# Kernel optimization log

Measured on AMD Instinct MI355X. Metric: run time of the kernel, lower is better.

The kernel has to match this reference:

```python
import jax, jax.numpy as jnp
import numpy as np

B, IN, H = 4096, 2048, 2048


def setup_inputs() -> dict:
    key = jax.random.key(0)
    ks = jax.random.split(key, 20)
    s_in = 1.0 / np.sqrt(IN)
    s_h = 1.0 / np.sqrt(H)
    inp = {
        "x": jax.random.normal(ks[0], (B, IN), jnp.float32),
        "h": jax.random.normal(ks[1], (B, H), jnp.float32),
        "c": jax.random.normal(ks[2], (B, H), jnp.float32),
    }
    names_in = [("Wii", "bii"), ("Wif", "bif"), ("Wig", "big"), ("Wio", "bio")]
    names_h = [("Whi", "bhi"), ("Whf", "bhf"), ("Whg", "bhg"), ("Who", "bho")]
    k = 3
    for wn, bn in names_in:
        inp[wn] = jax.random.normal(ks[k], (H, IN), jnp.float32) * s_in
        inp[bn] = jax.random.normal(ks[k + 1], (H,), jnp.float32) * s_in
        k += 2
    for wn, bn in names_h:
        inp[wn] = jax.random.normal(ks[k], (H, H), jnp.float32) * s_h
        inp[bn] = jax.random.normal(ks[k + 1], (H,), jnp.float32) * s_h
        k += 2
    return inp


def reference(x, h, c, Wii, bii, Whi, bhi, Wif, bif, Whf, bhf,
              Wig, big, Whg, bhg, Wio, bio, Who, bho):
    # Fuse the 4 input-projections and 4 hidden-projections into two GEMMs
    # (same math as 8 separate nn.Linear calls).
    Wx = jnp.concatenate([Wii, Wif, Wig, Wio], axis=0)   # [4H, IN]
    Wh = jnp.concatenate([Whi, Whf, Whg, Who], axis=0)   # [4H, H]
    bx = jnp.concatenate([bii, bif, big, bio])            # [4H]
    bh = jnp.concatenate([bhi, bhf, bhg, bho])            # [4H]
    gates = x @ Wx.T + h @ Wh.T + bx + bh                 # [B, 4H]
    ii, ff, gg, oo = jnp.split(gates, 4, axis=-1)
    i = jax.nn.sigmoid(ii)
    f = jax.nn.sigmoid(ff)
    g = jnp.tanh(gg)
    o = jax.nn.sigmoid(oo)
    c_new = f * c + i * g
    h_new = o * jnp.tanh(c_new)
    return jnp.stack([h_new, c_new])  # [2, B, H]
```

## Files before the change

kernel.cpp:

```cpp
#include <hip/hip_runtime.h>
#include <stdint.h>

typedef __attribute__((ext_vector_type(4))) float f32x4;
typedef __attribute__((ext_vector_type(8))) short bf16x8;

#define MFMA_BF16 __builtin_amdgcn_mfma_f32_16x16x32_bf16

__device__ __forceinline__ unsigned short f2bf(float f) {
  union { float f; uint32_t u; } a; a.f = f;
  uint32_t u = a.u;
  uint32_t r = (u + 0x7FFFu + ((u >> 16) & 1u)) >> 16;
  return (unsigned short)r;
}

__global__ void pack_a_kernel(const float4* __restrict__ x, const float4* __restrict__ hh,
                              ushort4* __restrict__ A) {
  const int total = 4096 * 1024;
  for (int q = blockIdx.x * blockDim.x + threadIdx.x; q < total; q += gridDim.x * blockDim.x) {
    int row = q >> 10, cq = q & 1023;
    float4 v = (cq < 512) ? x[row * 512 + cq] : hh[row * 512 + (cq - 512)];
    ushort4 o; o.x = f2bf(v.x); o.y = f2bf(v.y); o.z = f2bf(v.z); o.w = f2bf(v.w);
    A[q] = o;
  }
}

__global__ void pack_w_kernel(const float* __restrict__ Wii, const float* __restrict__ Wif,
                              const float* __restrict__ Wig, const float* __restrict__ Wio,
                              const float* __restrict__ Whi, const float* __restrict__ Whf,
                              const float* __restrict__ Whg, const float* __restrict__ Who,
                              ushort4* __restrict__ Wp) {
  const int total = 8192 * 1024;
  for (int q = blockIdx.x * blockDim.x + threadIdx.x; q < total; q += gridDim.x * blockDim.x) {
    int p = q >> 10, kq = q & 1023;
    int r = p & 255;
    int g = ((r >> 7) << 1) | ((r >> 4) & 1);
    int H = ((p >> 8) << 6) | (((r >> 5) & 3) << 4) | (r & 15);
    const float* src;
    if (kq < 512) src = (g == 0) ? Wii : (g == 1) ? Wif : (g == 2) ? Wig : Wio;
    else          src = (g == 0) ? Whi : (g == 1) ? Whf : (g == 2) ? Whg : Who;
    const float4 v = *(const float4*)&src[(size_t)H * 2048 + ((kq & 511) << 2)];
    ushort4 o; o.x = f2bf(v.x); o.y = f2bf(v.y); o.z = f2bf(v.z); o.w = f2bf(v.w);
    Wp[q] = o;
  }
}

#define STG(srcbase, jj, koff, dstE)                                                        \
  __builtin_amdgcn_global_load_lds(                                                        \
      (const __attribute__((address_space(1))) void*)((srcbase) + (size_t)(jj)*262144 + (koff)), \
      (__attribute__((address_space(3))) void*)(&smem[(dstE) + (jj)*4096]), 16, 0, 0)

__global__ __launch_bounds__(512, 1)
void lstm_gemm_kernel(const ushort* __restrict__ A, const ushort* __restrict__ Wp,
                      const float* __restrict__ c,
                      const float* __restrict__ bii, const float* __restrict__ bif_,
                      const float* __restrict__ big_, const float* __restrict__ bio_,
                      const float* __restrict__ bhi, const float* __restrict__ bhf,
                      const float* __restrict__ bhg, const float* __restrict__ bho,
                      float* __restrict__ out) {
  __shared__ ushort smem[65536];
  const int tid = threadIdx.x;
  const int lane = tid & 63, w = tid >> 6;
  const int wm = w >> 2, wn = w & 3;

  const int bid = blockIdx.x;
  const int xcd = bid & 7, q = bid >> 3;
  const int bn = (xcd << 2) | (q >> 4);
  const int bm = q & 15;

  const int laneRow = lane & 15, lane16 = lane >> 4;
  const int lr7 = laneRow & 7;
  const int colE0 = (lane16 ^ lr7) << 3;
  const int colE1 = ((4 + lane16) ^ lr7) << 3;

  const int srow = w * 8 + (lane >> 3);
  const int chunkOff = ((lane & 7) ^ (lane >> 3)) << 3;
  const ushort* aSrc = A + (size_t)(bm * 256 + srow) * 4096 + chunkOff;
  const ushort* bSrc = Wp + (size_t)(bn * 256 + srow) * 4096 + chunkOff;
  const int aDstW = w * 512;
  const int bDstW = 16384 + w * 512;

  const int aBase = (wm * 64 + laneRow) * 64;
  const int bBase = 16384 + (wn * 32 + laneRow) * 64;

  f32x4 acc[8][4];
#pragma unroll
  for (int i = 0; i < 8; i++)
#pragma unroll
    for (int j = 0; j < 4; j++) acc[i][j] = (f32x4){0.f, 0.f, 0.f, 0.f};

  STG(aSrc, 0, 0, aDstW); STG(aSrc, 1, 0, aDstW);
  STG(bSrc, 0, 0, bDstW); STG(bSrc, 1, 0, bDstW);
  STG(bSrc, 2, 0, bDstW); STG(bSrc, 3, 0, bDstW);
  STG(aSrc, 2, 0, aDstW); STG(aSrc, 3, 0, aDstW);
  STG(aSrc, 0, 64, 32768 + aDstW); STG(aSrc, 1, 64, 32768 + aDstW);
  STG(bSrc, 0, 64, 32768 + bDstW); STG(bSrc, 1, 64, 32768 + bDstW);
  STG(bSrc, 2, 64, 32768 + bDstW); STG(bSrc, 3, 64, 32768 + bDstW);
  STG(aSrc, 2, 64, 32768 + aDstW); STG(aSrc, 3, 64, 32768 + aDstW);
  asm volatile("s_waitcnt vmcnt(12)" ::: "memory");
  __builtin_amdgcn_s_barrier();
  __builtin_amdgcn_sched_barrier(0);

#pragma unroll 1
  for (int T = 0; T < 64; ++T) {
    const int bufE = (T & 1) << 15;
    const int kS = (T + 2) << 6;
    const bool st = (T <= 61);
    bf16x8 af[4][2], bf[4][2];

#pragma unroll
    for (int m = 0; m < 4; ++m) {
      af[m][0] = *(const bf16x8*)&smem[bufE + aBase + m * 1024 + colE0];
      af[m][1] = *(const bf16x8*)&smem[bufE + aBase + m * 1024 + colE1];
    }
#pragma unroll
    for (int n = 0; n < 2; ++n) {
      bf[n][0] = *(const bf16x8*)&smem[bufE + bBase + n * 1024 + colE0];
      bf[n][1] = *(const bf16x8*)&smem[bufE + bBase + n * 1024 + colE1];
    }
    __builtin_amdgcn_s_barrier();
    asm volatile("s_waitcnt lgkmcnt(0)" ::: "memory");
    __builtin_amdgcn_sched_barrier(0);
    __builtin_amdgcn_s_setprio(1);
#pragma unroll
    for (int m = 0; m < 4; ++m)
#pragma unroll
      for (int n = 0; n < 2; ++n) {
        acc[m][n] = MFMA_BF16(af[m][0], bf[n][0], acc[m][n], 0, 0, 0);
        acc[m][n] = MFMA_BF16(af[m][1], bf[n][1], acc[m][n], 0, 0, 0);
      }
    __builtin_amdgcn_s_setprio(0);
    if (T != 63) asm volatile("s_waitcnt vmcnt(10)" ::: "memory");
    else         asm volatile("s_waitcnt vmcnt(2)" ::: "memory");
    __builtin_amdgcn_s_barrier();

#pragma unroll
    for (int n = 0; n < 2; ++n) {
      bf[2 + n][0] = *(const bf16x8*)&smem[bufE + bBase + 8192 + n * 1024 + colE0];
      bf[2 + n][1] = *(const bf16x8*)&smem[bufE + bBase + 8192 + n * 1024 + colE1];
    }
    if (st) {
      STG(aSrc, 0, kS, bufE + aDstW); STG(aSrc, 1, kS, bufE + aDstW);
      STG(bSrc, 0, kS, bufE + bDstW); STG(bSrc, 1, kS, bufE + bDstW);
    }
    __builtin_amdgcn_s_barrier();
    asm volatile("s_waitcnt lgkmcnt(0)" ::: "memory");
    __builtin_amdgcn_sched_barrier(0);
    __builtin_amdgcn_s_setprio(1);
#pragma unroll
    for (int m = 0; m < 4; ++m)
#pragma unroll
      for (int n = 0; n < 2; ++n) {
        acc[m][2 + n] = MFMA_BF16(af[m][0], bf[2 + n][0], acc[m][2 + n], 0, 0, 0);
        acc[m][2 + n] = MFMA_BF16(af[m][1], bf[2 + n][1], acc[m][2 + n], 0, 0, 0);
      }
    __builtin_amdgcn_s_setprio(0);
    if (T != 63) asm volatile("s_waitcnt vmcnt(12)" ::: "memory");
    else         asm volatile("s_waitcnt vmcnt(0)" ::: "memory");
    __builtin_amdgcn_s_barrier();

#pragma unroll
    for (int m = 0; m < 4; ++m) {
      af[m][0] = *(const bf16x8*)&smem[bufE + aBase + 8192 + m * 1024 + colE0];
      af[m][1] = *(const bf16x8*)&smem[bufE + aBase + 8192 + m * 1024 + colE1];
    }
    if (st) { STG(bSrc, 2, kS, bufE + bDstW); STG(bSrc, 3, kS, bufE + bDstW); }
    __builtin_amdgcn_s_barrier();
    asm volatile("s_waitcnt lgkmcnt(0)" ::: "memory");
    __builtin_amdgcn_sched_barrier(0);
    __builtin_amdgcn_s_setprio(1);
#pragma unroll
    for (int m = 0; m < 4; ++m)
#pragma unroll
      for (int n = 0; n < 2; ++n) {
        acc[4 + m][n] = MFMA_BF16(af[m][0], bf[n][0], acc[4 + m][n], 0, 0, 0);
        acc[4 + m][n] = MFMA_BF16(af[m][1], bf[n][1], acc[4 + m][n], 0, 0, 0);
      }
    __builtin_amdgcn_s_setprio(0);
    __builtin_amdgcn_s_barrier();

    if (st) { STG(aSrc, 2, kS, bufE + aDstW); STG(aSrc, 3, kS, bufE + aDstW); }
    __builtin_amdgcn_s_barrier();
    __builtin_amdgcn_s_setprio(1);
#pragma unroll
    for (int m = 0; m < 4; ++m)
#pragma unroll
      for (int n = 0; n < 2; ++n) {
        acc[4 + m][2 + n] = MFMA_BF16(af[m][0], bf[2 + n][0], acc[4 + m][2 + n], 0, 0, 0);
        acc[4 + m][2 + n] = MFMA_BF16(af[m][1], bf[2 + n][1], acc[4 + m][2 + n], 0, 0, 0);
      }
    __builtin_amdgcn_s_setprio(0);
    if (T < 63) {
      if (T != 62) asm volatile("s_waitcnt vmcnt(12)" ::: "memory");
      else         asm volatile("s_waitcnt vmcnt(4)" ::: "memory");
      __builtin_amdgcn_s_barrier();
      __builtin_amdgcn_sched_barrier(0);
    }
  }

  const int hcol = bn * 64 + wn * 16 + laneRow;
  const float bI = bii[hcol] + bhi[hcol];
  const float bF = bif_[hcol] + bhf[hcol];
  const float bG = big_[hcol] + bhg[hcol];
  const float bO = bio_[hcol] + bho[hcol];
#pragma unroll
  for (int mi = 0; mi < 8; ++mi) {
    const int rowBase = bm * 256 + (mi >> 2) * 128 + wm * 64 + (mi & 3) * 16 + lane16 * 4;
#pragma unroll
    for (int rr = 0; rr < 4; ++rr) {
      const int row = rowBase + rr;
      const float ii = acc[mi][0][rr] + bI;
      const float ff = acc[mi][1][rr] + bF;
      const float gg = acc[mi][2][rr] + bG;
      const float oo = acc[mi][3][rr] + bO;
      const float iv = 1.f / (1.f + __expf(-ii));
      const float fv = 1.f / (1.f + __expf(-ff));
      const float gv = tanhf(gg);
      const float ov = 1.f / (1.f + __expf(-oo));
      const float cv = c[(size_t)row * 2048 + hcol];
      const float cn = fv * cv + iv * gv;
      const float hn = ov * tanhf(cn);
      out[(size_t)row * 2048 + hcol] = hn;
      out[(size_t)8388608 + (size_t)row * 2048 + hcol] = cn;
    }
  }
}

extern "C" void kernel_launch(void* const* d_in, const int* in_sizes, int n_in,
                              void* d_out, int out_size, void* d_ws, size_t ws_size,
                              hipStream_t stream) {
  const float* x = (const float*)d_in[0];
  const float* h = (const float*)d_in[1];
  const float* c = (const float*)d_in[2];
  const float* Wii = (const float*)d_in[3];  const float* bii = (const float*)d_in[4];
  const float* Wif = (const float*)d_in[5];  const float* bif_ = (const float*)d_in[6];
  const float* Wig = (const float*)d_in[7];  const float* big_ = (const float*)d_in[8];
  const float* Wio = (const float*)d_in[9];  const float* bio_ = (const float*)d_in[10];
  const float* Whi = (const float*)d_in[11]; const float* bhi = (const float*)d_in[12];
  const float* Whf = (const float*)d_in[13]; const float* bhf = (const float*)d_in[14];
  const float* Whg = (const float*)d_in[15]; const float* bhg = (const float*)d_in[16];
  const float* Who = (const float*)d_in[17]; const float* bho = (const float*)d_in[18];

  ushort* Abf = (ushort*)d_ws;
  ushort* Wpk = Abf + (size_t)4096 * 4096;
  float* out = (float*)d_out;

  pack_a_kernel<<<2048, 256, 0, stream>>>((const float4*)x, (const float4*)h, (ushort4*)Abf);
  pack_w_kernel<<<2048, 256, 0, stream>>>(Wii, Wif, Wig, Wio, Whi, Whf, Whg, Who, (ushort4*)Wpk);
  lstm_gemm_kernel<<<512, 512, 0, stream>>>(Abf, Wpk, c,
                                            bii, bif_, big_, bio_, bhi, bhf, bhg, bho, out);
}
```

Baseline: 334.3 us.

## Software-pipeline LDS fragment reads across K-tiles with register double buffering

Restructures the main GEMM loop so the LDS reads for the next K-tile's first A/B fragments are issued during the current tile's later MFMA phases, using ping-pong register buffers and a 2x unrolled loop. Explicit lgkmcnt(0) waits and extra barriers between LDS reads and MFMAs are removed, relying on compiler-inserted waits, and vmcnt thresholds are retuned to the new global-load ordering. This aims to hide LDS latency behind matrix math and cut barrier stalls, at the cost of more live vector registers and tighter correctness reliance on barrier/vmcnt placement.

```diff
diff --git a/kernel.cpp b/kernel.cpp
--- a/kernel.cpp
+++ b/kernel.cpp
@@ -49,6 +49,87 @@
       (const __attribute__((address_space(1))) void*)((srcbase) + (size_t)(jj)*262144 + (koff)), \
       (__attribute__((address_space(3))) void*)(&smem[(dstE) + (jj)*4096]), 16, 0, 0)
 
+#define TILE_BODY(T_, bufE_, AF0c, BF01c, AF0n, BF01n)                                      \
+  {                                                                                         \
+    const int kS = ((T_) + 2) << 6;                                                         \
+    const bool st = (T_) <= 61;                                                             \
+    const bool rdn = (T_) < 63;                                                             \
+                 \
+    _Pragma("unroll") for (int n = 0; n < 2; ++n) {                                         \
+      bf23_[n][0] = *(const bf16x8*)&smem[(bufE_) + bBase + 8192 + n * 1024 + colE0];       \
+      bf23_[n][1] = *(const bf16x8*)&smem[(bufE_) + bBase + 8192 + n * 1024 + colE1];       \
+    }                                                                                       \
+    __builtin_amdgcn_s_setprio(1);                                                          \
+    _Pragma("unroll") for (int m = 0; m < 4; ++m)                                           \
+      _Pragma("unroll") for (int n = 0; n < 2; ++n) {                                       \
+        acc[m][n] = MFMA_BF16(AF0c[m][0], BF01c[n][0], acc[m][n], 0, 0, 0);                 \
+        acc[m][n] = MFMA_BF16(AF0c[m][1], BF01c[n][1], acc[m][n], 0, 0, 0);                 \
+      }                                                                                     \
+    __builtin_amdgcn_s_setprio(0);                                                          \
+    if ((T_) < 63) asm volatile("s_waitcnt vmcnt(8)" ::: "memory");                         \
+    else           asm volatile("s_waitcnt vmcnt(0)" ::: "memory");                         \
+    __builtin_amdgcn_sched_barrier(0);                                                      \
+    __builtin_amdgcn_s_barrier();                                                           \
+            \
+    _Pragma("unroll") for (int m = 0; m < 4; ++m) {                                         \
+      af1_[m][0] = *(const bf16x8*)&smem[(bufE_) + aBase + 8192 + m * 1024 + colE0];        \
+      af1_[m][1] = *(const bf16x8*)&smem[(bufE_) + aBase + 8192 + m * 1024 + colE1];        \
+    }                                                                                       \
+    if (st) {                                                                               \
+      STG(aSrc, 0, kS, (bufE_) + aDstW); STG(aSrc, 1, kS, (bufE_) + aDstW);                 \
+      STG(bSrc, 0, kS, (bufE_) + bDstW); STG(bSrc, 1, kS, (bufE_) + bDstW);                 \
+    }                                                                                       \
+    __builtin_amdgcn_s_setprio(1);                                                          \
+    _Pragma("unroll") for (int m = 0; m < 4; ++m)                                           \
+      _Pragma("unroll") for (int n = 0; n < 2; ++n) {                                       \
+        acc[m][2 + n] = MFMA_BF16(AF0c[m][0], bf23_[n][0], acc[m][2 + n], 0, 0, 0);         \
+        acc[m][2 + n] = MFMA_BF16(AF0c[m][1], bf23_[n][1], acc[m][2 + n], 0, 0, 0);         \
+      }                                                                                     \
+    __builtin_amdgcn_s_setprio(0);                                                          \
+    if ((T_) < 62)       asm volatile("s_waitcnt vmcnt(8)" ::: "memory");                   \
+    else if ((T_) == 62) asm volatile("s_waitcnt vmcnt(4)" ::: "memory");                   \
+    __builtin_amdgcn_sched_barrier(0);                                                      \
+    __builtin_amdgcn_s_barrier();                                                           \
+     \
+    if (rdn) {                                                                              \
+      _Pragma("unroll") for (int m = 0; m < 4; ++m) {                                       \
+        AF0n[m][0] = *(const bf16x8*)&smem[((bufE_) ^ 32768) + aBase + m * 1024 + colE0];   \
+        AF0n[m][1] = *(const bf16x8*)&smem[((bufE_) ^ 32768) + aBase + m * 1024 + colE1];   \
+      }                                                                                     \
+    }                                                                                       \
+    if (st) { STG(bSrc, 2, kS, (bufE_) + bDstW); STG(bSrc, 3, kS, (bufE_) + bDstW); }       \
+    __builtin_amdgcn_s_setprio(1);                                                          \
+    _Pragma("unroll") for (int m = 0; m < 4; ++m)                                           \
+      _Pragma("unroll") for (int n = 0; n < 2; ++n) {                                       \
+        acc[4 + m][n] = MFMA_BF16(af1_[m][0], BF01c[n][0], acc[4 + m][n], 0, 0, 0);         \
+        acc[4 + m][n] = MFMA_BF16(af1_[m][1], BF01c[n][1], acc[4 + m][n], 0, 0, 0);         \
+      }                                                                                     \
+    __builtin_amdgcn_s_setprio(0);                                                          \
+    __builtin_amdgcn_sched_barrier(0);                                                      \
+    __builtin_amdgcn_s_barrier();                                                           \
+           \
+    if (rdn) {                                                                              \
+      _Pragma("unroll") for (int n = 0; n < 2; ++n) {                                       \
+        BF01n[n][0] = *(const bf16x8*)&smem[((bufE_) ^ 32768) + bBase + n * 1024 + colE0];  \
+        BF01n[n][1] = *(const bf16x8*)&smem[((bufE_) ^ 32768) + bBase + n * 1024 + colE1];  \
+      }                                                                                     \
+    }                                                                                       \
+    if (st) { STG(aSrc, 2, kS, (bufE_) + aDstW); STG(aSrc, 3, kS, (bufE_) + aDstW); }       \
+    __builtin_amdgcn_s_setprio(1);                                                          \
+    _Pragma("unroll") for (int m = 0; m < 4; ++m)                                           \
+      _Pragma("unroll") for (int n = 0; n < 2; ++n) {                                       \
+        acc[4 + m][2 + n] = MFMA_BF16(af1_[m][0], bf23_[n][0], acc[4 + m][2 + n], 0, 0, 0); \
+        acc[4 + m][2 + n] = MFMA_BF16(af1_[m][1], bf23_[n][1], acc[4 + m][2 + n], 0, 0, 0); \
+      }                                                                                     \
+    __builtin_amdgcn_s_setprio(0);                                                          \
+    if ((T_) < 62)       asm volatile("s_waitcnt vmcnt(10)" ::: "memory");                  \
+    else if ((T_) == 62) asm volatile("s_waitcnt vmcnt(2)" ::: "memory");                   \
+    if ((T_) < 63) {                                                                        \
+      __builtin_amdgcn_sched_barrier(0);                                                    \
+      __builtin_amdgcn_s_barrier();                                                         \
+    }                                                                                       \
+  }
+
 __global__ __launch_bounds__(512, 1)
 void lstm_gemm_kernel(const ushort* __restrict__ A, const ushort* __restrict__ Wp,
                       const float* __restrict__ c,
@@ -96,105 +177,27 @@
   STG(bSrc, 0, 64, 32768 + bDstW); STG(bSrc, 1, 64, 32768 + bDstW);
   STG(bSrc, 2, 64, 32768 + bDstW); STG(bSrc, 3, 64, 32768 + bDstW);
   STG(aSrc, 2, 64, 32768 + aDstW); STG(aSrc, 3, 64, 32768 + aDstW);
-  asm volatile("s_waitcnt vmcnt(12)" ::: "memory");
+  asm volatile("s_waitcnt vmcnt(10)" ::: "memory");
   __builtin_amdgcn_s_barrier();
   __builtin_amdgcn_sched_barrier(0);
 
+  bf16x8 af0A[4][2], af0B[4][2], bf01A[4][2], bf01B[4][2], af1_[4][2], bf23_[4][2];
+#pragma unroll
+  for (int m = 0; m < 4; ++m) {
+    af0A[m][0] = *(const bf16x8*)&smem[aBase + m * 1024 + colE0];
+    af0A[m][1] = *(const bf16x8*)&smem[aBase + m * 1024 + colE1];
+  }
+#pragma unroll
+  for (int n = 0; n < 2; ++n) {
+    bf01A[n][0] = *(const bf16x8*)&smem[bBase + n * 1024 + colE0];
+    bf01A[n][1] = *(const bf16x8*)&smem[bBase + n * 1024 + colE1];
+  }
+
 #pragma unroll 1
-  for (int T = 0; T < 64; ++T) {
-    const int bufE = (T & 1) << 15;
-    const int kS = (T + 2) << 6;
-    const bool st = (T <= 61);
-    bf16x8 af[4][2], bf[4][2];
-
-#pragma unroll
-    for (int m = 0; m < 4; ++m) {
-      af[m][0] = *(const bf16x8*)&smem[bufE + aBase + m * 1024 + colE0];
-      af[m][1] = *(const bf16x8*)&smem[bufE + aBase + m * 1024 + colE1];
-    }
-#pragma unroll
-    for (int n = 0; n < 2; ++n) {
-      bf[n][0] = *(const bf16x8*)&smem[bufE + bBase + n * 1024 + colE0];
-      bf[n][1] = *(const bf16x8*)&smem[bufE + bBase + n * 1024 + colE1];
-    }
-    __builtin_amdgcn_s_barrier();
-    asm volatile("s_waitcnt lgkmcnt(0)" ::: "memory");
-    __builtin_amdgcn_sched_barrier(0);
-    __builtin_amdgcn_s_setprio(1);
-#pragma unroll
-    for (int m = 0; m < 4; ++m)
-#pragma unroll
-      for (int n = 0; n < 2; ++n) {
-        acc[m][n] = MFMA_BF16(af[m][0], bf[n][0], acc[m][n], 0, 0, 0);
-        acc[m][n] = MFMA_BF16(af[m][1], bf[n][1], acc[m][n], 0, 0, 0);
-      }
-    __builtin_amdgcn_s_setprio(0);
-    if (T != 63) asm volatile("s_waitcnt vmcnt(10)" ::: "memory");
-    else         asm volatile("s_waitcnt vmcnt(2)" ::: "memory");
-    __builtin_amdgcn_s_barrier();
-
-#pragma unroll
-    for (int n = 0; n < 2; ++n) {
-      bf[2 + n][0] = *(const bf16x8*)&smem[bufE + bBase + 8192 + n * 1024 + colE0];
-      bf[2 + n][1] = *(const bf16x8*)&smem[bufE + bBase + 8192 + n * 1024 + colE1];
-    }
-    if (st) {
-      STG(aSrc, 0, kS, bufE + aDstW); STG(aSrc, 1, kS, bufE + aDstW);
-      STG(bSrc, 0, kS, bufE + bDstW); STG(bSrc, 1, kS, bufE + bDstW);
-    }
-    __builtin_amdgcn_s_barrier();
-    asm volatile("s_waitcnt lgkmcnt(0)" ::: "memory");
-    __builtin_amdgcn_sched_barrier(0);
-    __builtin_amdgcn_s_setprio(1);
-#pragma unroll
-    for (int m = 0; m < 4; ++m)
-#pragma unroll
-      for (int n = 0; n < 2; ++n) {
-        acc[m][2 + n] = MFMA_BF16(af[m][0], bf[2 + n][0], acc[m][2 + n], 0, 0, 0);
-        acc[m][2 + n] = MFMA_BF16(af[m][1], bf[2 + n][1], acc[m][2 + n], 0, 0, 0);
-      }
-    __builtin_amdgcn_s_setprio(0);
-    if (T != 63) asm volatile("s_waitcnt vmcnt(12)" ::: "memory");
-    else         asm volatile("s_waitcnt vmcnt(0)" ::: "memory");
-    __builtin_amdgcn_s_barrier();
-
-#pragma unroll
-    for (int m = 0; m < 4; ++m) {
-      af[m][0] = *(const bf16x8*)&smem[bufE + aBase + 8192 + m * 1024 + colE0];
-      af[m][1] = *(const bf16x8*)&smem[bufE + aBase + 8192 + m * 1024 + colE1];
-    }
-    if (st) { STG(bSrc, 2, kS, bufE + bDstW); STG(bSrc, 3, kS, bufE + bDstW); }
-    __builtin_amdgcn_s_barrier();
-    asm volatile("s_waitcnt lgkmcnt(0)" ::: "memory");
-    __builtin_amdgcn_sched_barrier(0);
-    __builtin_amdgcn_s_setprio(1);
-#pragma unroll
-    for (int m = 0; m < 4; ++m)
-#pragma unroll
-      for (int n = 0; n < 2; ++n) {
-        acc[4 + m][n] = MFMA_BF16(af[m][0], bf[n][0], acc[4 + m][n], 0, 0, 0);
-        acc[4 + m][n] = MFMA_BF16(af[m][1], bf[n][1], acc[4 + m][n], 0, 0, 0);
-      }
-    __builtin_amdgcn_s_setprio(0);
-    __builtin_amdgcn_s_barrier();
-
-    if (st) { STG(aSrc, 2, kS, bufE + aDstW); STG(aSrc, 3, kS, bufE + aDstW); }
-    __builtin_amdgcn_s_barrier();
-    __builtin_amdgcn_s_setprio(1);
-#pragma unroll
-    for (int m = 0; m < 4; ++m)
-#pragma unroll
-      for (int n = 0; n < 2; ++n) {
-        acc[4 + m][2 + n] = MFMA_BF16(af[m][0], bf[2 + n][0], acc[4 + m][2 + n], 0, 0, 0);
-        acc[4 + m][2 + n] = MFMA_BF16(af[m][1], bf[2 + n][1], acc[4 + m][2 + n], 0, 0, 0);
-      }
-    __builtin_amdgcn_s_setprio(0);
-    if (T < 63) {
-      if (T != 62) asm volatile("s_waitcnt vmcnt(12)" ::: "memory");
-      else         asm volatile("s_waitcnt vmcnt(4)" ::: "memory");
-      __builtin_amdgcn_s_barrier();
-      __builtin_amdgcn_sched_barrier(0);
-    }
+  for (int t = 0; t < 32; ++t) {
+    const int Ta = 2 * t, Tb = 2 * t + 1;
+    TILE_BODY(Ta, 0,     af0A, bf01A, af0B, bf01B);
+    TILE_BODY(Tb, 32768, af0B, bf01B, af0A, bf01A);
   }
 
   const int hcol = bn * 64 + wn * 16 + laneRow;
```

Measured after the change: 1.293 ms. 287% more time.
